# Performance work log

Hardware: AMD Instinct MI355X
Metric: run time of the kernel (lower is better)

The kernel has to match this reference:

```python
import jax, jax.numpy as jnp
import numpy as np

MARGIN = 1.0
EPS = 1e-6  # F.pairwise_distance adds eps to the elementwise diff


def setup_inputs() -> dict:
    key = jax.random.key(0)
    k1, k2, k3 = jax.random.split(key, 3)
    N, D = 8192, 64
    anchor_embeddings = jax.random.normal(k1, (N, D), dtype=jnp.float32)
    positive_embeddings = jax.random.normal(k2, (N, D), dtype=jnp.float32)
    labels = jax.random.randint(k3, (N,), 0, 2, dtype=jnp.int64)
    return {
        "anchor_embeddings": anchor_embeddings,
        "positive_embeddings": positive_embeddings,
        "labels": labels,
    }


def _pairwise_dist(a, p):
    # dist[i, j] = ||(a_i + eps) - p_j||_2, matching F.pairwise_distance's
    # norm(x1 - x2 + eps). Computed via the Gram trick to avoid an [N,N,D]
    # intermediate.
    a = a + EPS
    a2 = jnp.sum(a * a, axis=-1)                      # [N]
    p2 = jnp.sum(p * p, axis=-1)                      # [N]
    sq = a2[:, None] + p2[None, :] - 2.0 * (a @ p.T)  # [N, N]
    return jnp.sqrt(jnp.maximum(sq, 1e-12))


def reference(anchor_embeddings, positive_embeddings, labels):
    N = anchor_embeddings.shape[0]
    dist = _pairwise_dist(anchor_embeddings, positive_embeddings)  # [N, N]
    pos_dist = jnp.diagonal(dist)                                  # [N], d(a_i, p_i)
    hinge = jax.nn.relu(pos_dist[:, None] - dist + MARGIN)         # [N, N]
    # pair (i, j) contributes iff labels[i] == 1 and i != j
    row_mask = (labels == 1)[:, None]
    offdiag = ~jnp.eye(N, dtype=bool)
    mask = (row_mask & offdiag).astype(hinge.dtype)
    count = jnp.sum(mask)
    total = jnp.sum(hinge * mask)
    return jnp.where(count > 0, total / jnp.maximum(count, 1.0), 0.0)
```

## Files before the change

kernel.cpp:

```cpp
#include <hip/hip_runtime.h>
#include <hip/hip_bf16.h>

#define NROWS 8192
#define DDIM 64
#define MARGIN_F 1.0f
#define EPS_F 1e-6f


typedef __attribute__((ext_vector_type(8))) short bf16x8;
typedef __attribute__((ext_vector_type(4))) float f32x4;

static __device__ __forceinline__ unsigned short f2bf(float x) {
    __hip_bfloat16 h = __float2bfloat16(x);
    return *reinterpret_cast<unsigned short*>(&h);
}

__global__ __launch_bounds__(256) void
prep_kernel(const float* __restrict__ A, const float* __restrict__ P,
            unsigned short* __restrict__ Abf, unsigned short* __restrict__ Pbf,
            float* __restrict__ a2g, float* __restrict__ pdg,
            float* __restrict__ p2g) {
    int t   = threadIdx.x;
    int gid = blockIdx.x * 256 + t;
    int row = gid >> 4;
    int c4  = (gid & 15) * 4;
    float4 a = *(const float4*)&A[row * DDIM + c4];
    float4 p = *(const float4*)&P[row * DDIM + c4];
    a.x += EPS_F; a.y += EPS_F; a.z += EPS_F; a.w += EPS_F;
    ushort4 ab, pb;
    ab.x = f2bf(a.x); ab.y = f2bf(a.y); ab.z = f2bf(a.z); ab.w = f2bf(a.w);
    pb.x = f2bf(p.x); pb.y = f2bf(p.y); pb.z = f2bf(p.z); pb.w = f2bf(p.w);
    *(ushort4*)&Abf[row * DDIM + c4] = ab;
    *(ushort4*)&Pbf[row * DDIM + c4] = pb;
    float va2 = a.x*a.x + a.y*a.y + a.z*a.z + a.w*a.w;
    float vp2 = p.x*p.x + p.y*p.y + p.z*p.z + p.w*p.w;
    float vap = a.x*p.x + a.y*p.y + a.z*p.z + a.w*p.w;
    #pragma unroll
    for (int off = 8; off; off >>= 1) {
        va2 += __shfl_xor(va2, off);
        vp2 += __shfl_xor(vp2, off);
        vap += __shfl_xor(vap, off);
    }
    if ((t & 15) == 0) {
        a2g[row] = va2;
        p2g[row] = vp2;
        float sq = fmaxf(va2 + vp2 - 2.0f * vap, 1e-12f);
        pdg[row] = sqrtf(sq) + MARGIN_F;
    }
}

__global__ __launch_bounds__(256) void
compact_kernel(const int* __restrict__ labels, int* __restrict__ sel,
               int* __restrict__ cnt) {
    __shared__ int lab[256 * 33];
    __shared__ int scan[256];
    int t = threadIdx.x;
    #pragma unroll
    for (int i = 0; i < 32; ++i) {
        int j = i * 256 + t;
        lab[(j >> 5) * 33 + (j & 31)] = labels[j];
    }
    __syncthreads();
    int lc = 0;
    #pragma unroll
    for (int i = 0; i < 32; ++i) lc += (lab[t * 33 + i] == 1) ? 1 : 0;
    scan[t] = lc;
    __syncthreads();
    for (int off = 1; off < 256; off <<= 1) {
        int v = (t >= off) ? scan[t - off] : 0;
        __syncthreads();
        if (t >= off) scan[t] += v;
        __syncthreads();
    }
    int o = scan[t] - lc;
    for (int i = 0; i < 32; ++i) {
        if (lab[t * 33 + i] == 1) sel[o++] = t * 32 + i;
    }
    if (t == 255) *cnt = scan[255];
}

__global__ __launch_bounds__(256) void
main_kernel(const unsigned short* __restrict__ Abf, const unsigned short* __restrict__ Pbf,
            const float* __restrict__ a2g, const float* __restrict__ pdg,
            const float* __restrict__ p2g, const int* __restrict__ sel,
            const int* __restrict__ cnt, float* __restrict__ partial) {
    __shared__ float sA2[128], sPd[128], sP2[128];
    __shared__ int   sGi[128];
    __shared__ float wsum[4];

    int M = *cnt;
    int row0 = blockIdx.y * 128;
    int col0 = blockIdx.x * 128;
    int bid  = blockIdx.y * 64 + blockIdx.x;
    int t = threadIdx.x;
    if (row0 >= M) { if (t == 0) partial[bid] = 0.0f; return; }

    if (t < 128) {
        int gi = sel[min(row0 + t, M - 1)];
        sGi[t] = gi;
        sA2[t] = a2g[gi];
        sPd[t] = pdg[gi];
        sP2[t] = p2g[col0 + t];
    }
    __syncthreads();

    int wid  = t >> 6;
    int lane = t & 63;
    int wm = (wid >> 1) * 64;
    int wn = (wid & 1) * 64;
    int lm   = lane & 15;
    int quad = lane >> 4;

    bf16x8 af[2][4], bg[2][4];
    #pragma unroll
    for (int a = 0; a < 4; ++a) {
        const unsigned short* pa = Abf + (size_t)sGi[wm + a * 16 + lm] * DDIM + quad * 8;
        af[0][a] = *(const bf16x8*)pa;
        af[1][a] = *(const bf16x8*)(pa + 32);
    }
    #pragma unroll
    for (int b = 0; b < 4; ++b) {
        const unsigned short* pb = Pbf + (size_t)(col0 + wn + b * 16 + lm) * DDIM + quad * 8;
        bg[0][b] = *(const bf16x8*)pb;
        bg[1][b] = *(const bf16x8*)(pb + 32);
    }

    f32x4 acc[4][4] = {};
    #pragma unroll
    for (int s = 0; s < 2; ++s)
        #pragma unroll
        for (int a = 0; a < 4; ++a)
            #pragma unroll
            for (int b = 0; b < 4; ++b)
                acc[a][b] = __builtin_amdgcn_mfma_f32_16x16x32_bf16(af[s][a], bg[s][b], acc[a][b], 0, 0, 0);

    float bsum = 0.0f;
    #pragma unroll
    for (int a = 0; a < 4; ++a) {
        #pragma unroll
        for (int r = 0; r < 4; ++r) {
            int il = wm + a * 16 + quad * 4 + r;
            bool valid = (row0 + il) < M;
            float ra2 = sA2[il];
            float rpd = sPd[il];
            int   gi  = sGi[il];
            #pragma unroll
            for (int b = 0; b < 4; ++b) {
                int jl = wn + b * 16 + lm;
                int j  = col0 + jl;
                float sq = fmaxf(ra2 + sP2[jl] - 2.0f * acc[a][b][r], 1e-12f);
                float h  = rpd - sqrtf(sq);
                if (valid && (gi != j) && (h > 0.0f)) bsum += h;
            }
        }
    }

    #pragma unroll
    for (int off = 32; off; off >>= 1) bsum += __shfl_xor(bsum, off);
    if (lane == 0) wsum[wid] = bsum;
    __syncthreads();
    if (t == 0) partial[bid] = wsum[0] + wsum[1] + wsum[2] + wsum[3];
}

__global__ __launch_bounds__(256) void
finalize_kernel(const int* __restrict__ cnt, const float* __restrict__ partial,
                float* __restrict__ out) {
    __shared__ float wsum[4];
    int t = threadIdx.x;
    const float4* p4 = (const float4*)partial;
    float s = 0.0f;
    #pragma unroll
    for (int i = 0; i < 4; ++i) {
        float4 v = p4[i * 256 + t];
        s += v.x + v.y + v.z + v.w;
    }
    #pragma unroll
    for (int off = 32; off; off >>= 1) s += __shfl_xor(s, off);
    if ((t & 63) == 0) wsum[t >> 6] = s;
    __syncthreads();
    if (t == 0) {
        int M = *cnt;
        float tot = wsum[0] + wsum[1] + wsum[2] + wsum[3];
        float c = (float)M * (float)(NROWS - 1);
        out[0] = (M > 0) ? tot / c : 0.0f;
    }
}

extern "C" void kernel_launch(void* const* d_in, const int* in_sizes, int n_in,
                              void* d_out, int out_size, void* d_ws, size_t ws_size,
                              hipStream_t stream) {
    const float* A      = (const float*)d_in[0];
    const float* P      = (const float*)d_in[1];
    const int*   labels = (const int*)d_in[2];
    float* out = (float*)d_out;

    char* ws = (char*)d_ws;
    unsigned short* Abf = (unsigned short*)(ws);
    unsigned short* Pbf = (unsigned short*)(ws + (1 << 20));
    float* a2g     = (float*)(ws + (2 << 20));
    float* pdg     = (float*)(ws + (2 << 20) + 32768);
    float* p2g     = (float*)(ws + (2 << 20) + 65536);
    int*   sel     = (int*)(ws + (2 << 20) + 98304);
    int*   cnt     = (int*)(ws + (2 << 20) + 131072);
    float* partial = (float*)(ws + (2 << 20) + 135168);

    prep_kernel<<<dim3(NROWS * 16 / 256), dim3(256), 0, stream>>>(A, P, Abf, Pbf, a2g, pdg, p2g);
    compact_kernel<<<dim3(1), dim3(256), 0, stream>>>(labels, sel, cnt);

    dim3 grid(NROWS / 128, NROWS / 128);
    main_kernel<<<grid, dim3(256), 0, stream>>>(Abf, Pbf, a2g, pdg, p2g, sel, cnt, partial);

    finalize_kernel<<<1, dim3(256), 0, stream>>>(cnt, partial, out);
}
```

Baseline: 96.60 us.

## Fuse prep and compaction kernels, move diagonal exclusion to finalize, simplify epilogue

Merges the prep and label-compaction kernels into one launch, with the extra block running the scan alongside the conversion blocks. The main kernel's per-element diagonal check (gi != j) and its branch are removed. Instead, each row's diagonal hinge, computed from the same bf16 operands, is subtracted in finalize. The epilogue becomes branch-free: it uses fma, a fast hardware sqrt, a multiply-by-mask for row validity, hoisted sP2 loads, and P fragment loads moved before the barrier. The risks are that the bf16 diagonal correction may not exactly cancel the MFMA result, and that dropping the 1e-12 clamp before the sqrt can yield NaN when the squared distance goes negative from rounding.

```diff
diff --git a/kernel.cpp b/kernel.cpp
--- a/kernel.cpp
+++ b/kernel.cpp
@@ -14,69 +14,77 @@
     __hip_bfloat16 h = __float2bfloat16(x);
     return *reinterpret_cast<unsigned short*>(&h);
 }
+static __device__ __forceinline__ float bf2f(unsigned short u) {
+    return __uint_as_float(((unsigned)u) << 16);
+}
 
 __global__ __launch_bounds__(256) void
-prep_kernel(const float* __restrict__ A, const float* __restrict__ P,
-            unsigned short* __restrict__ Abf, unsigned short* __restrict__ Pbf,
-            float* __restrict__ a2g, float* __restrict__ pdg,
-            float* __restrict__ p2g) {
-    int t   = threadIdx.x;
-    int gid = blockIdx.x * 256 + t;
-    int row = gid >> 4;
-    int c4  = (gid & 15) * 4;
-    float4 a = *(const float4*)&A[row * DDIM + c4];
-    float4 p = *(const float4*)&P[row * DDIM + c4];
-    a.x += EPS_F; a.y += EPS_F; a.z += EPS_F; a.w += EPS_F;
-    ushort4 ab, pb;
-    ab.x = f2bf(a.x); ab.y = f2bf(a.y); ab.z = f2bf(a.z); ab.w = f2bf(a.w);
-    pb.x = f2bf(p.x); pb.y = f2bf(p.y); pb.z = f2bf(p.z); pb.w = f2bf(p.w);
-    *(ushort4*)&Abf[row * DDIM + c4] = ab;
-    *(ushort4*)&Pbf[row * DDIM + c4] = pb;
-    float va2 = a.x*a.x + a.y*a.y + a.z*a.z + a.w*a.w;
-    float vp2 = p.x*p.x + p.y*p.y + p.z*p.z + p.w*p.w;
-    float vap = a.x*p.x + a.y*p.y + a.z*p.z + a.w*p.w;
-    #pragma unroll
-    for (int off = 8; off; off >>= 1) {
-        va2 += __shfl_xor(va2, off);
-        vp2 += __shfl_xor(vp2, off);
-        vap += __shfl_xor(vap, off);
-    }
-    if ((t & 15) == 0) {
-        a2g[row] = va2;
-        p2g[row] = vp2;
-        float sq = fmaxf(va2 + vp2 - 2.0f * vap, 1e-12f);
-        pdg[row] = sqrtf(sq) + MARGIN_F;
-    }
-}
-
-__global__ __launch_bounds__(256) void
-compact_kernel(const int* __restrict__ labels, int* __restrict__ sel,
-               int* __restrict__ cnt) {
+prep_compact_kernel(const float* __restrict__ A, const float* __restrict__ P,
+                    const int* __restrict__ labels,
+                    unsigned short* __restrict__ Abf, unsigned short* __restrict__ Pbf,
+                    float* __restrict__ a2g, float* __restrict__ pdg,
+                    float* __restrict__ p2g, float* __restrict__ hdg,
+                    int* __restrict__ sel, int* __restrict__ cnt) {
     __shared__ int lab[256 * 33];
     __shared__ int scan[256];
     int t = threadIdx.x;
-    #pragma unroll
-    for (int i = 0; i < 32; ++i) {
-        int j = i * 256 + t;
-        lab[(j >> 5) * 33 + (j & 31)] = labels[j];
-    }
-    __syncthreads();
-    int lc = 0;
-    #pragma unroll
-    for (int i = 0; i < 32; ++i) lc += (lab[t * 33 + i] == 1) ? 1 : 0;
-    scan[t] = lc;
-    __syncthreads();
-    for (int off = 1; off < 256; off <<= 1) {
-        int v = (t >= off) ? scan[t - off] : 0;
+
+    if (blockIdx.x < 512) {
+        int gid = blockIdx.x * 256 + t;
+        int row = gid >> 4;
+        int c4  = (gid & 15) * 4;
+        float4 a = *(const float4*)&A[row * DDIM + c4];
+        float4 p = *(const float4*)&P[row * DDIM + c4];
+        a.x += EPS_F; a.y += EPS_F; a.z += EPS_F; a.w += EPS_F;
+        ushort4 ab, pb;
+        ab.x = f2bf(a.x); ab.y = f2bf(a.y); ab.z = f2bf(a.z); ab.w = f2bf(a.w);
+        pb.x = f2bf(p.x); pb.y = f2bf(p.y); pb.z = f2bf(p.z); pb.w = f2bf(p.w);
+        *(ushort4*)&Abf[row * DDIM + c4] = ab;
+        *(ushort4*)&Pbf[row * DDIM + c4] = pb;
+        float va2 = a.x*a.x + a.y*a.y + a.z*a.z + a.w*a.w;
+        float vp2 = p.x*p.x + p.y*p.y + p.z*p.z + p.w*p.w;
+        float vap = a.x*p.x + a.y*p.y + a.z*p.z + a.w*p.w;
+        float vdd = bf2f(ab.x)*bf2f(pb.x) + bf2f(ab.y)*bf2f(pb.y)
+                  + bf2f(ab.z)*bf2f(pb.z) + bf2f(ab.w)*bf2f(pb.w);
+        #pragma unroll
+        for (int off = 8; off; off >>= 1) {
+            va2 += __shfl_xor(va2, off);
+            vp2 += __shfl_xor(vp2, off);
+            vap += __shfl_xor(vap, off);
+            vdd += __shfl_xor(vdd, off);
+        }
+        if ((t & 15) == 0) {
+            a2g[row] = va2;
+            p2g[row] = vp2;
+            float pd = sqrtf(fmaxf(va2 + vp2 - 2.0f * vap, 1e-12f)) + MARGIN_F;
+            pdg[row] = pd;
+            float sqd = fmaxf(va2 + vp2 - 2.0f * vdd, 1e-12f);
+            hdg[row] = fmaxf(pd - __builtin_amdgcn_sqrtf(sqd), 0.0f);
+        }
+    } else {
+        #pragma unroll
+        for (int i = 0; i < 32; ++i) {
+            int j = i * 256 + t;
+            lab[(j >> 5) * 33 + (j & 31)] = labels[j];
+        }
         __syncthreads();
-        if (t >= off) scan[t] += v;
+        int lc = 0;
+        #pragma unroll
+        for (int i = 0; i < 32; ++i) lc += (lab[t * 33 + i] == 1) ? 1 : 0;
+        scan[t] = lc;
         __syncthreads();
-    }
-    int o = scan[t] - lc;
-    for (int i = 0; i < 32; ++i) {
-        if (lab[t * 33 + i] == 1) sel[o++] = t * 32 + i;
-    }
-    if (t == 255) *cnt = scan[255];
+        for (int off = 1; off < 256; off <<= 1) {
+            int v = (t >= off) ? scan[t - off] : 0;
+            __syncthreads();
+            if (t >= off) scan[t] += v;
+            __syncthreads();
+        }
+        int o = scan[t] - lc;
+        for (int i = 0; i < 32; ++i) {
+            if (lab[t * 33 + i] == 1) sel[o++] = t * 32 + i;
+        }
+        if (t == 255) *cnt = scan[255];
+    }
 }
 
 __global__ __launch_bounds__(256) void
@@ -89,11 +97,26 @@
     __shared__ float wsum[4];
 
     int M = *cnt;
-    int row0 = blockIdx.y * 128;
-    int col0 = blockIdx.x * 128;
-    int bid  = blockIdx.y * 64 + blockIdx.x;
+    int row0 = blockIdx.y << 7;
+    int col0 = blockIdx.x << 7;
+    int bid  = (blockIdx.y << 6) + blockIdx.x;
     int t = threadIdx.x;
     if (row0 >= M) { if (t == 0) partial[bid] = 0.0f; return; }
+
+    int wid  = t >> 6;
+    int lane = t & 63;
+    int wm   = (wid >> 1) << 6;
+    int wn   = (wid & 1) << 6;
+    int lm   = lane & 15;
+    int quad = lane >> 4;
+
+    bf16x8 bg[2][4];
+    #pragma unroll
+    for (int b = 0; b < 4; ++b) {
+        const unsigned short* pb = Pbf + (size_t)(col0 + wn + b * 16 + lm) * DDIM + quad * 8;
+        bg[0][b] = *(const bf16x8*)pb;
+        bg[1][b] = *(const bf16x8*)(pb + 32);
+    }
 
     if (t < 128) {
         int gi = sel[min(row0 + t, M - 1)];
@@ -104,26 +127,13 @@
     }
     __syncthreads();
 
-    int wid  = t >> 6;
-    int lane = t & 63;
-    int wm = (wid >> 1) * 64;
-    int wn = (wid & 1) * 64;
-    int lm   = lane & 15;
-    int quad = lane >> 4;
-
-    bf16x8 af[2][4], bg[2][4];
+    bf16x8 af[2][4];
     #pragma unroll
     for (int a = 0; a < 4; ++a) {
         const unsigned short* pa = Abf + (size_t)sGi[wm + a * 16 + lm] * DDIM + quad * 8;
         af[0][a] = *(const bf16x8*)pa;
         af[1][a] = *(const bf16x8*)(pa + 32);
     }
-    #pragma unroll
-    for (int b = 0; b < 4; ++b) {
-        const unsigned short* pb = Pbf + (size_t)(col0 + wn + b * 16 + lm) * DDIM + quad * 8;
-        bg[0][b] = *(const bf16x8*)pb;
-        bg[1][b] = *(const bf16x8*)(pb + 32);
-    }
 
     f32x4 acc[4][4] = {};
     #pragma unroll
@@ -134,23 +144,24 @@
             for (int b = 0; b < 4; ++b)
                 acc[a][b] = __builtin_amdgcn_mfma_f32_16x16x32_bf16(af[s][a], bg[s][b], acc[a][b], 0, 0, 0);
 
+    float spv[4];
+    #pragma unroll
+    for (int b = 0; b < 4; ++b) spv[b] = sP2[wn + b * 16 + lm];
+
     float bsum = 0.0f;
     #pragma unroll
     for (int a = 0; a < 4; ++a) {
         #pragma unroll
         for (int r = 0; r < 4; ++r) {
             int il = wm + a * 16 + quad * 4 + r;
-            bool valid = (row0 + il) < M;
+            float rm  = ((row0 + il) < M) ? 1.0f : 0.0f;
             float ra2 = sA2[il];
             float rpd = sPd[il];
-            int   gi  = sGi[il];
             #pragma unroll
             for (int b = 0; b < 4; ++b) {
-                int jl = wn + b * 16 + lm;
-                int j  = col0 + jl;
-                float sq = fmaxf(ra2 + sP2[jl] - 2.0f * acc[a][b][r], 1e-12f);
-                float h  = rpd - sqrtf(sq);
-                if (valid && (gi != j) && (h > 0.0f)) bsum += h;
+                float sq = fmaf(-2.0f, acc[a][b][r], ra2 + spv[b]);
+                float h  = rpd - __builtin_amdgcn_sqrtf(sq);
+                bsum = fmaf(fmaxf(h, 0.0f), rm, bsum);
             }
         }
     }
@@ -164,6 +175,7 @@
 
 __global__ __launch_bounds__(256) void
 finalize_kernel(const int* __restrict__ cnt, const float* __restrict__ partial,
+                const float* __restrict__ hdg, const int* __restrict__ sel,
                 float* __restrict__ out) {
     __shared__ float wsum[4];
     int t = threadIdx.x;
@@ -174,12 +186,13 @@
         float4 v = p4[i * 256 + t];
         s += v.x + v.y + v.z + v.w;
     }
+    int M = *cnt;
+    for (int idx = t; idx < M; idx += 256) s -= hdg[sel[idx]];
     #pragma unroll
     for (int off = 32; off; off >>= 1) s += __shfl_xor(s, off);
     if ((t & 63) == 0) wsum[t >> 6] = s;
     __syncthreads();
     if (t == 0) {
-        int M = *cnt;
         float tot = wsum[0] + wsum[1] + wsum[2] + wsum[3];
         float c = (float)M * (float)(NROWS - 1);
         out[0] = (M > 0) ? tot / c : 0.0f;
@@ -203,12 +216,13 @@
     int*   sel     = (int*)(ws + (2 << 20) + 98304);
     int*   cnt     = (int*)(ws + (2 << 20) + 131072);
     float* partial = (float*)(ws + (2 << 20) + 135168);
-
-    prep_kernel<<<dim3(NROWS * 16 / 256), dim3(256), 0, stream>>>(A, P, Abf, Pbf, a2g, pdg, p2g);
-    compact_kernel<<<dim3(1), dim3(256), 0, stream>>>(labels, sel, cnt);
+    float* hdg     = (float*)(ws + (2 << 20) + 151552);
+
+    prep_compact_kernel<<<dim3(513), dim3(256), 0, stream>>>(A, P, labels, Abf, Pbf,
+                                                             a2g, pdg, p2g, hdg, sel, cnt);
 
     dim3 grid(NROWS / 128, NROWS / 128);
     main_kernel<<<grid, dim3(256), 0, stream>>>(Abf, Pbf, a2g, pdg, p2g, sel, cnt, partial);
 
-    finalize_kernel<<<1, dim3(256), 0, stream>>>(cnt, partial, out);
-}
+    finalize_kernel<<<1, dim3(256), 0, stream>>>(cnt, partial, hdg, sel, out);
+}
```

Measured after the change: 89.96 us. 6.9% less time.
